# Kernel optimization log

Hardware: AMD Instinct MI355X
Metric: run time of the kernel (lower is better)

## Reference

```python
import jax, jax.numpy as jnp
import numpy as np

D_MODEL = 1024
NUM_HEADS = 16
D_K = D_MODEL // NUM_HEADS
THETA = 10000.0
BATCH = 2
SEQ = 2048


def setup_inputs() -> dict:
    key = jax.random.key(0)
    ks = jax.random.split(key, 5)
    std = np.sqrt(2.0 / (D_MODEL + D_MODEL))
    return {
        "x": jax.random.normal(ks[0], (BATCH, SEQ, D_MODEL), dtype=jnp.float32),
        "Wq": jax.random.normal(ks[1], (D_MODEL, D_MODEL), dtype=jnp.float32) * std,
        "Wk": jax.random.normal(ks[2], (D_MODEL, D_MODEL), dtype=jnp.float32) * std,
        "Wv": jax.random.normal(ks[3], (D_MODEL, D_MODEL), dtype=jnp.float32) * std,
        "Wo": jax.random.normal(ks[4], (D_MODEL, D_MODEL), dtype=jnp.float32) * std,
        "token_positions": jnp.arange(SEQ, dtype=jnp.int64),
    }


def _apply_rope(t, cos, sin):
    # t: [B, H, S, D_K]; cos/sin: [S, D_K//2]
    # Block-diag 2x2 rotation on consecutive pairs (2k, 2k+1) == elementwise rotation.
    tr = t.reshape(*t.shape[:-1], D_K // 2, 2)
    t0, t1 = tr[..., 0], tr[..., 1]
    o0 = t0 * cos - t1 * sin
    o1 = t0 * sin + t1 * cos
    return jnp.stack([o0, o1], axis=-1).reshape(t.shape)


def reference(x, Wq, Wk, Wv, Wo, token_positions):
    B, S, _ = x.shape
    # projections: custom Linear does x @ W.T
    def split_heads(t):
        return t.reshape(B, S, NUM_HEADS, D_K).transpose(0, 2, 1, 3)  # [B,H,S,Dk]

    q = split_heads(x @ Wq.T)
    k = split_heads(x @ Wk.T)
    v = split_heads(x @ Wv.T)

    # RoPE angle table: theta_ik = pos / THETA**(2k/d_k)
    inv_freq = 1.0 / (THETA ** (2.0 * jnp.arange(D_K // 2, dtype=jnp.float32) / D_K))
    angles = token_positions.astype(jnp.float32)[:, None] * inv_freq[None, :]  # [S, Dk//2]
    cos, sin = jnp.cos(angles), jnp.sin(angles)

    q = _apply_rope(q, cos, sin)
    k = _apply_rope(k, cos, sin)

    scale = 1.0 / np.sqrt(D_K)
    scores = jnp.einsum("bhqd,bhkd->bhqk", q, k) * scale  # [B,H,S,S]
    causal = jnp.tril(jnp.ones((S, S), dtype=bool))
    scores = jnp.where(causal, scores, -jnp.inf)
    attn = jax.nn.softmax(scores, axis=-1)
    out = jnp.einsum("bhqk,bhkd->bhqd", attn, v)  # [B,H,S,Dk]
    out = out.transpose(0, 2, 1, 3).reshape(B, S, D_MODEL)
    return out @ Wo.T
```

## Files before the change

### kernel.cpp

```cpp
#include <hip/hip_runtime.h>
#include <hip/hip_bf16.h>
#include <cstdint>
#include <cstddef>

#define BATCH 2
#define SEQ   2048
#define DM    1024
#define NH    16
#define DK    64
#define LOG2E 1.4426950408889634f

typedef __attribute__((ext_vector_type(8)))  short short8;
typedef __attribute__((ext_vector_type(4)))  float f32x4;
typedef __attribute__((ext_vector_type(16))) float f32x16;
typedef __attribute__((ext_vector_type(4)))  int   i32x4;
typedef __attribute__((ext_vector_type(2)))  int   i32x2;

__device__ __forceinline__ void gload_lds16(const __hip_bfloat16* g, __hip_bfloat16* l) {
  __builtin_amdgcn_global_load_lds((const __attribute__((address_space(1))) void*)g,
                                   (__attribute__((address_space(3))) void*)l, 16, 0, 0);
}

__device__ __forceinline__ int cvtpk_bf16(float lo, float hi) {
  int r;
  asm("v_cvt_pk_bf16_f32 %0, %1, %2" : "=v"(r) : "v"(lo), "v"(hi));
  return r;
}

__device__ __forceinline__ float bf2f(short v) {
  return __int_as_float(((int)(unsigned short)v) << 16);
}

__device__ __forceinline__ float partner32(float x, int hi) {
  auto r = __builtin_amdgcn_permlane32_swap(__float_as_int(x), __float_as_int(x), false, false);
  return __int_as_float(hi ? r[0] : r[1]);
}

__global__ void cast_all(const float* __restrict__ x,  const float* __restrict__ Wq,
                         const float* __restrict__ Wk, const float* __restrict__ Wv,
                         const float* __restrict__ Wo, __hip_bfloat16* __restrict__ dst,
                         const int* __restrict__ pos,  float2* __restrict__ tbl) {
  const int NX = BATCH * SEQ * DM;
  int t = blockIdx.x * 256 + threadIdx.x;
  if (t < SEQ * 32) {
    int s = t >> 5, d2 = t & 31;
    float ang = (float)pos[s] * exp2f(-(float)d2 * 0.415241011860920f);
    float cv, sv;
    __sincosf(ang, &sv, &cv);
    tbl[t] = make_float2(cv, sv);
  }
  size_t i = (size_t)t * 4;
  const float* s;
  if (i < (size_t)NX) {
    s = x + i;
  } else {
    size_t j = i - NX;
    int wsel = (int)(j >> 20);
    size_t o = j & ((1u << 20) - 1);
    s = (wsel == 0 ? Wq : wsel == 1 ? Wk : wsel == 2 ? Wv : Wo) + o;
  }
  float4 v = *(const float4*)s;
  i32x2 pk;
  pk[0] = cvtpk_bf16(v.x, v.y);
  pk[1] = cvtpk_bf16(v.z, v.w);
  *(i32x2*)(dst + i) = pk;
}

template<bool F32OUT, bool VSPLIT>
__global__ __launch_bounds__(256)
void gemm_bt(const __hip_bfloat16* __restrict__ A,
             const __hip_bfloat16* __restrict__ Bw,
             void* __restrict__ Cv, __hip_bfloat16* __restrict__ vt,
             int M, int N, int K, int ldc) {
  __shared__ __hip_bfloat16 As[2][128 * 32];
  __shared__ __hip_bfloat16 Bs[2][128 * 32];
  const int tid  = threadIdx.x;
  const int lane = tid & 63;
  const int w    = tid >> 6;
  const int wr   = w >> 1, wc = w & 1;
  const int g    = lane >> 4;
  const int lr   = lane & 15;

  const int nwg = gridDim.x * gridDim.y;
  const int bid = blockIdx.y * gridDim.x + blockIdx.x;
  const int cpx = nwg >> 3;
  const int sbid = (bid & 7) * cpx + (bid >> 3);
  const int bx = sbid % gridDim.x, by = sbid / gridDim.x;
  const int bm0  = by * 128;
  const int bn0  = bx * 128;

  f32x4 acc[4][4] = {};

  const int strow = lane >> 2;
  const int stcol = (lane & 3) * 8;

  auto STAGE = [&](int buf, int kt) {
    #pragma unroll
    for (int it = 0; it < 2; ++it) {
      int row = (w * 2 + it) * 16 + strow;
      gload_lds16(A  + (size_t)(bm0 + row) * K + kt + stcol, &As[buf][row * 32 + stcol]);
      gload_lds16(Bw + (size_t)(bn0 + row) * K + kt + stcol, &Bs[buf][row * 32 + stcol]);
    }
  };

  STAGE(0, 0);
  __syncthreads();
  int cur = 0;
  const int nk = K / 32;
  for (int ki = 0; ki < nk; ++ki) {
    if (ki + 1 < nk) STAGE(cur ^ 1, (ki + 1) * 32);
    short8 a[4], b[4];
    #pragma unroll
    for (int m = 0; m < 4; ++m)
      a[m] = *(const short8*)(&As[cur][(wr * 64 + m * 16 + lr) * 32 + g * 8]);
    #pragma unroll
    for (int n = 0; n < 4; ++n)
      b[n] = *(const short8*)(&Bs[cur][(wc * 64 + n * 16 + lr) * 32 + g * 8]);
    #pragma unroll
    for (int m = 0; m < 4; ++m)
      #pragma unroll
      for (int n = 0; n < 4; ++n)
        acc[m][n] = __builtin_amdgcn_mfma_f32_16x16x32_bf16(a[m], b[n], acc[m][n], 0, 0, 0);
    __syncthreads();
    cur ^= 1;
  }

  if (VSPLIT && bn0 >= 2048) {
    #pragma unroll
    for (int m = 0; m < 4; ++m)
      #pragma unroll
      for (int n = 0; n < 4; ++n) {
        int nn = bn0 + wc * 64 + n * 16 + lr - 2048;
        int hd = nn >> 6, d = nn & 63;
        int m0 = bm0 + wr * 64 + m * 16 + g * 4;
        int bb = m0 >> 11, ss = m0 & 2047;
        i32x2 pk;
        pk[0] = cvtpk_bf16(acc[m][n][0], acc[m][n][1]);
        pk[1] = cvtpk_bf16(acc[m][n][2], acc[m][n][3]);
        *(i32x2*)(vt + ((size_t)(bb * NH + hd) * DK + d) * SEQ + ss) = pk;
      }
  } else {
    #pragma unroll
    for (int m = 0; m < 4; ++m)
      #pragma unroll
      for (int n = 0; n < 4; ++n) {
        int col = bn0 + wc * 64 + n * 16 + lr;
        #pragma unroll
        for (int r = 0; r < 4; ++r) {
          int row = bm0 + wr * 64 + m * 16 + g * 4 + r;
          float v = acc[m][n][r];
          if (F32OUT) ((float*)Cv)[(size_t)row * ldc + col] = v;
          else        ((__hip_bfloat16*)Cv)[(size_t)row * ldc + col] = __float2bfloat16(v);
        }
      }
  }
}

__global__ void rope_vec(__hip_bfloat16* __restrict__ qk, const float2* __restrict__ tbl) {
  int idx = blockIdx.x * 256 + threadIdx.x;
  int row = idx >> 7;
  int hg  = idx & 127;
  int h   = hg >> 3, gg = hg & 7;
  const float QS = 0.125f * LOG2E;
  size_t base = (size_t)row * 2048 + h * 64 + gg * 8;
  const float2* tp = tbl + (row & (SEQ - 1)) * 32 + gg * 4;
  short8 q = *(const short8*)(qk + base);
  short8 k = *(const short8*)(qk + base + 1024);
  i32x4 qo, ko;
  #pragma unroll
  for (int j = 0; j < 4; ++j) {
    float2 cs = tp[j];
    float q0 = bf2f(q[2 * j]), q1 = bf2f(q[2 * j + 1]);
    float k0 = bf2f(k[2 * j]), k1 = bf2f(k[2 * j + 1]);
    qo[j] = cvtpk_bf16((q0 * cs.x - q1 * cs.y) * QS, (q0 * cs.y + q1 * cs.x) * QS);
    ko[j] = cvtpk_bf16(k0 * cs.x - k1 * cs.y,        k0 * cs.y + k1 * cs.x);
  }
  *(i32x4*)(qk + base)        = qo;
  *(i32x4*)(qk + base + 1024) = ko;
}

__global__ __launch_bounds__(512)
void flash_attn(const __hip_bfloat16* __restrict__ qk,
                const __hip_bfloat16* __restrict__ vt,
                __hip_bfloat16* __restrict__ outb) {
  __shared__ __hip_bfloat16 Kls[2][64 * 64];
  __shared__ __hip_bfloat16 Vls[2][64 * 64];
  const int pi = blockIdx.x;
  const int NQB = SEQ / 128;
  const int qbh = NQB - 1 - pi, qbl = pi;
  const int hd = blockIdx.y, b = blockIdx.z;
  const int tid = threadIdx.x, lane = tid & 63, w = tid >> 6;
  const int wh = w & 3;
  const int qb_eff = (w < 4) ? qbh : qbl;
  const int hi = lane >> 5, ql = lane & 31;
  const int q0w = qb_eff * 128 + wh * 32;
  const int nt  = 2 * qbh + 2;
  const int tmaxw = 2 * qb_eff + (wh >> 1);

  const __hip_bfloat16* Qb = qk + (size_t)(b * SEQ) * 2048 + hd * DK;
  const __hip_bfloat16* Kg = qk + (size_t)(b * SEQ) * 2048 + 1024 + hd * DK;
  const __hip_bfloat16* Vg = vt + (size_t)(b * NH + hd) * DK * SEQ;

  short8 qf[4];
  #pragma unroll
  for (int c = 0; c < 4; ++c)
    qf[c] = *(const short8*)(Qb + (size_t)(q0w + ql) * 2048 + c * 16 + hi * 8);

  f32x16 o0 = {}, o1 = {};
  float m_run = -1e30f, l_run = 0.f;

  const int srow = tid >> 3;
  const int sc0  = (tid & 7) * 8;
  const int swz  = (srow & 7) << 3;

  short8 kr, vr;
  kr = *(const short8*)(Kg + (size_t)srow * 2048 + sc0);
  vr = *(const short8*)(Vg + (size_t)srow * SEQ + sc0);
  *(short8*)(&Kls[0][srow * 64 + (sc0 ^ swz)]) = kr;
  *(short8*)(&Vls[0][srow * 64 + (sc0 ^ swz)]) = vr;

  for (int t = 0; t < nt; ++t) {
    const int cur = t & 1;
    if (t + 1 < nt) {
      int r0 = (t + 1) * 64;
      kr = *(const short8*)(Kg + (size_t)(r0 + srow) * 2048 + sc0);
      vr = *(const short8*)(Vg + (size_t)srow * SEQ + r0 + sc0);
    }
    __syncthreads();

    if (t <= tmaxw) {
      f32x16 s0 = {}, s1 = {};
      __builtin_amdgcn_s_setprio(1);
      #pragma unroll
      for (int c = 0; c < 4; ++c) {
        int col = (c * 16 + hi * 8) ^ ((ql & 7) << 3);
        short8 ka = *(const short8*)(&Kls[cur][ql * 64 + col]);
        short8 kb = *(const short8*)(&Kls[cur][(32 + ql) * 64 + col]);
        s0 = __builtin_amdgcn_mfma_f32_32x32x16_bf16(ka, qf[c], s0, 0, 0, 0);
        s1 = __builtin_amdgcn_mfma_f32_32x32x16_bf16(kb, qf[c], s1, 0, 0, 0);
      }
      __builtin_amdgcn_s_setprio(0);

      if (t * 64 + 63 > q0w) {
        int qg = q0w + ql;
        #pragma unroll
        for (int r = 0; r < 16; ++r) {
          int krow = (r & 3) + 8 * (r >> 2) + 4 * hi;
          if (t * 64 + krow > qg)      s0[r] = -1e30f;
          if (t * 64 + 32 + krow > qg) s1[r] = -1e30f;
        }
      }

      float mx = s0[0];
      #pragma unroll
      for (int r = 1; r < 16; ++r) mx = fmaxf(mx, s0[r]);
      #pragma unroll
      for (int r = 0; r < 16; ++r) mx = fmaxf(mx, s1[r]);
      mx = fmaxf(mx, partner32(mx, hi));

      if (!__all(mx <= m_run + 8.f)) {
        float mn  = fmaxf(m_run, mx);
        float fac = __builtin_amdgcn_exp2f(m_run - mn);
        m_run = mn;
        l_run *= fac;
        #pragma unroll
        for (int r = 0; r < 16; ++r) { o0[r] *= fac; o1[r] *= fac; }
      }
      float sum = 0.f;
      #pragma unroll
      for (int r = 0; r < 16; ++r) { s0[r] = __builtin_amdgcn_exp2f(s0[r] - m_run); sum += s0[r]; }
      #pragma unroll
      for (int r = 0; r < 16; ++r) { s1[r] = __builtin_amdgcn_exp2f(s1[r] - m_run); sum += s1[r]; }
      sum += partner32(sum, hi);
      l_run += sum;

      short8 pf[4];
      #pragma unroll
      for (int kt = 0; kt < 2; ++kt) {
        const f32x16& sv = kt ? s1 : s0;
        #pragma unroll
        for (int u = 0; u < 2; ++u) {
          int wa0 = cvtpk_bf16(sv[8 * u + 0], sv[8 * u + 1]);
          int wa1 = cvtpk_bf16(sv[8 * u + 2], sv[8 * u + 3]);
          int wb0 = cvtpk_bf16(sv[8 * u + 4], sv[8 * u + 5]);
          int wb1 = cvtpk_bf16(sv[8 * u + 6], sv[8 * u + 7]);
          auto r0 = __builtin_amdgcn_permlane32_swap(wa0, wb0, false, false);
          auto r1 = __builtin_amdgcn_permlane32_swap(wa1, wb1, false, false);
          i32x4 fr; fr[0] = r0[0]; fr[1] = r1[0]; fr[2] = r0[1]; fr[3] = r1[1];
          pf[kt * 2 + u] = *(short8*)&fr;
        }
      }

      __builtin_amdgcn_s_setprio(1);
      #pragma unroll
      for (int cc = 0; cc < 4; ++cc) {
        int col = (cc * 16 + hi * 8) ^ ((ql & 7) << 3);
        short8 va = *(const short8*)(&Vls[cur][ql * 64 + col]);
        short8 vb = *(const short8*)(&Vls[cur][(32 + ql) * 64 + col]);
        o0 = __builtin_amdgcn_mfma_f32_32x32x16_bf16(va, pf[cc], o0, 0, 0, 0);
        o1 = __builtin_amdgcn_mfma_f32_32x32x16_bf16(vb, pf[cc], o1, 0, 0, 0);
      }
      __builtin_amdgcn_s_setprio(0);
    }

    if (t + 1 < nt) {
      const int nxt = cur ^ 1;
      *(short8*)(&Kls[nxt][srow * 64 + (sc0 ^ swz)]) = kr;
      *(short8*)(&Vls[nxt][srow * 64 + (sc0 ^ swz)]) = vr;
    }
  }

  float inv = 1.f / l_run;
  __hip_bfloat16* orow = outb + (size_t)(b * SEQ + q0w + ql) * DM + hd * DK;
  #pragma unroll
  for (int dt = 0; dt < 2; ++dt) {
    const f32x16& oa = dt ? o1 : o0;
    #pragma unroll
    for (int a = 0; a < 4; ++a) {
      int d0 = dt * 32 + a * 8 + hi * 4;
      i32x2 pk;
      pk[0] = cvtpk_bf16(oa[4 * a + 0] * inv, oa[4 * a + 1] * inv);
      pk[1] = cvtpk_bf16(oa[4 * a + 2] * inv, oa[4 * a + 3] * inv);
      *(i32x2*)(orow + d0) = pk;
    }
  }
}

extern "C" void kernel_launch(void* const* d_in, const int* in_sizes, int n_in,
                              void* d_out, int out_size, void* d_ws, size_t ws_size,
                              hipStream_t stream) {
  const float* x  = (const float*)d_in[0];
  const float* Wq = (const float*)d_in[1];
  const float* Wk = (const float*)d_in[2];
  const float* Wv = (const float*)d_in[3];
  const float* Wo = (const float*)d_in[4];
  const int*   tp = (const int*)d_in[5];
  float* out = (float*)d_out;

  char* ws = (char*)d_ws;
  __hip_bfloat16* xb    = (__hip_bfloat16*)(ws);
  __hip_bfloat16* wqkv  = (__hip_bfloat16*)(ws + (8u  << 20));
  __hip_bfloat16* wob   = (__hip_bfloat16*)(ws + (14u << 20));
  __hip_bfloat16* qkbuf = (__hip_bfloat16*)(ws + (16u << 20));
  __hip_bfloat16* vtbuf = (__hip_bfloat16*)(ws + (32u << 20));
  __hip_bfloat16* attnb = (__hip_bfloat16*)(ws + (40u << 20));
  float2*         tbl   = (float2*)(ws + (40u << 20));

  cast_all<<<8192, 256, 0, stream>>>(x, Wq, Wk, Wv, Wo, xb, tp, tbl);

  gemm_bt<false, true><<<dim3(3 * DM / 128, BATCH * SEQ / 128), 256, 0, stream>>>(
      xb, wqkv, (void*)qkbuf, vtbuf, BATCH * SEQ, 3 * DM, DM, 2048);

  rope_vec<<<(BATCH * SEQ * NH * 8) / 256, 256, 0, stream>>>(qkbuf, tbl);

  flash_attn<<<dim3(SEQ / 256, NH, BATCH), 512, 0, stream>>>(qkbuf, vtbuf, attnb);

  gemm_bt<true, false><<<dim3(DM / 128, BATCH * SEQ / 128), 256, 0, stream>>>(
      attnb, wob, (void*)out, nullptr, BATCH * SEQ, DM, DM, DM);
}
```

Baseline: 116.8 us.

## Split paired causal flash-attention blocks into single-qblock 256-thread blocks

```diff
diff --git a/kernel.cpp b/kernel.cpp
--- a/kernel.cpp
+++ b/kernel.cpp
@@ -179,23 +179,24 @@
   *(i32x4*)(qk + base + 1024) = ko;
 }
 
-__global__ __launch_bounds__(512)
+__global__ __launch_bounds__(256)
 void flash_attn(const __hip_bfloat16* __restrict__ qk,
                 const __hip_bfloat16* __restrict__ vt,
                 __hip_bfloat16* __restrict__ outb) {
   __shared__ __hip_bfloat16 Kls[2][64 * 64];
   __shared__ __hip_bfloat16 Vls[2][64 * 64];
-  const int pi = blockIdx.x;
-  const int NQB = SEQ / 128;
-  const int qbh = NQB - 1 - pi, qbl = pi;
-  const int hd = blockIdx.y, b = blockIdx.z;
+  const int sid  = blockIdx.x;
+  const int half = sid >> 8;
+  const int rem  = sid & 255;
+  const int hd   = rem >> 4;
+  const int i16  = rem & 15;
+  const int qb   = half ? i16 : 15 - i16;
+  const int b    = half;
   const int tid = threadIdx.x, lane = tid & 63, w = tid >> 6;
-  const int wh = w & 3;
-  const int qb_eff = (w < 4) ? qbh : qbl;
   const int hi = lane >> 5, ql = lane & 31;
-  const int q0w = qb_eff * 128 + wh * 32;
-  const int nt  = 2 * qbh + 2;
-  const int tmaxw = 2 * qb_eff + (wh >> 1);
+  const int q0w = qb * 128 + w * 32;
+  const int nt  = 2 * qb + 2;
+  const int tmaxw = 2 * qb + (w >> 1);
 
   const __hip_bfloat16* Qb = qk + (size_t)(b * SEQ) * 2048 + hd * DK;
   const __hip_bfloat16* Kg = qk + (size_t)(b * SEQ) * 2048 + 1024 + hd * DK;
@@ -211,21 +212,29 @@
 
   const int srow = tid >> 3;
   const int sc0  = (tid & 7) * 8;
-  const int swz  = (srow & 7) << 3;
-
-  short8 kr, vr;
-  kr = *(const short8*)(Kg + (size_t)srow * 2048 + sc0);
-  vr = *(const short8*)(Vg + (size_t)srow * SEQ + sc0);
-  *(short8*)(&Kls[0][srow * 64 + (sc0 ^ swz)]) = kr;
-  *(short8*)(&Vls[0][srow * 64 + (sc0 ^ swz)]) = vr;
+
+  short8 kr0, kr1, vr0, vr1;
+  auto LOAD = [&](int t) {
+    int r0 = t * 64;
+    kr0 = *(const short8*)(Kg + (size_t)(r0 + srow) * 2048 + sc0);
+    kr1 = *(const short8*)(Kg + (size_t)(r0 + 32 + srow) * 2048 + sc0);
+    vr0 = *(const short8*)(Vg + (size_t)srow * SEQ + r0 + sc0);
+    vr1 = *(const short8*)(Vg + (size_t)(32 + srow) * SEQ + r0 + sc0);
+  };
+  auto WRITE = [&](int buf) {
+    int r1 = srow + 32;
+    *(short8*)(&Kls[buf][srow * 64 + (sc0 ^ ((srow & 7) << 3))]) = kr0;
+    *(short8*)(&Kls[buf][r1 * 64 + (sc0 ^ ((r1 & 7) << 3))])     = kr1;
+    *(short8*)(&Vls[buf][srow * 64 + (sc0 ^ ((srow & 7) << 3))]) = vr0;
+    *(short8*)(&Vls[buf][r1 * 64 + (sc0 ^ ((r1 & 7) << 3))])     = vr1;
+  };
+
+  LOAD(0);
+  WRITE(0);
 
   for (int t = 0; t < nt; ++t) {
     const int cur = t & 1;
-    if (t + 1 < nt) {
-      int r0 = (t + 1) * 64;
-      kr = *(const short8*)(Kg + (size_t)(r0 + srow) * 2048 + sc0);
-      vr = *(const short8*)(Vg + (size_t)srow * SEQ + r0 + sc0);
-    }
+    if (t + 1 < nt) LOAD(t + 1);
     __syncthreads();
 
     if (t <= tmaxw) {
@@ -303,11 +312,7 @@
       __builtin_amdgcn_s_setprio(0);
     }
 
-    if (t + 1 < nt) {
-      const int nxt = cur ^ 1;
-      *(short8*)(&Kls[nxt][srow * 64 + (sc0 ^ swz)]) = kr;
-      *(short8*)(&Vls[nxt][srow * 64 + (sc0 ^ swz)]) = vr;
-    }
+    if (t + 1 < nt) WRITE(cur ^ 1);
   }
 
   float inv = 1.f / l_run;
@@ -353,7 +358,7 @@
 
   rope_vec<<<(BATCH * SEQ * NH * 8) / 256, 256, 0, stream>>>(qkbuf, tbl);
 
-  flash_attn<<<dim3(SEQ / 256, NH, BATCH), 512, 0, stream>>>(qkbuf, vtbuf, attnb);
+  flash_attn<<<512, 256, 0, stream>>>(qkbuf, vtbuf, attnb);
 
   gemm_bt<true, false><<<dim3(DM / 128, BATCH * SEQ / 128), 256, 0, stream>>>(
       attnb, wob, (void*)out, nullptr, BATCH * SEQ, DM, DM, DM);
```

Result: slower. 124.9 us (+6.9%).
